# Performance work log

Hardware: AMD Instinct MI355X
Metric: run time of the kernel (lower is better)

## Reference

```python
import jax, jax.numpy as jnp
import numpy as np
import math

EPS_NORM = 1e-12
BN_EPS = 1e-5


def _l2norm(x):
    n = jnp.sqrt(jnp.sum(x * x, axis=-1, keepdims=True))
    return x / jnp.maximum(n, EPS_NORM)


def setup_inputs() -> dict:
    key = jax.random.key(0)
    ks = jax.random.split(key, 16)
    b, c, t, l = 16, 32, 16, 256
    s = 0.05
    return {
        "x": jax.random.normal(ks[0], (b, c, t, l), jnp.float32),
        "q_w": jax.random.normal(ks[1], (c, c), jnp.float32) * s,
        "q_b": jax.random.normal(ks[2], (c,), jnp.float32) * s,
        "k_w": jax.random.normal(ks[3], (c, c), jnp.float32) * s,
        "k_b": jax.random.normal(ks[4], (c,), jnp.float32) * s,
        "v_w": jax.random.normal(ks[5], (c, c), jnp.float32) * s,
        "v_b": jax.random.normal(ks[6], (c,), jnp.float32) * s,
        "m_w": jax.random.normal(ks[7], (c, c), jnp.float32) * s,
        "m_b": jax.random.normal(ks[8], (c,), jnp.float32) * s,
        "pre_prompt": jax.random.normal(ks[9], (1, c, 1, l), jnp.float32) * s,
        "conv_w": jax.random.normal(ks[10], (c, c, 9, 1), jnp.float32) * s,
        "conv_b": jax.random.normal(ks[11], (c,), jnp.float32) * s,
        "bn_gamma": jnp.ones((c,), jnp.float32),
        "bn_beta": jnp.zeros((c,), jnp.float32),
        "lin_w": jax.random.normal(ks[12], (l, l), jnp.float32) * s,
        "lin_b": jax.random.normal(ks[13], (l,), jnp.float32) * s,
        "atten_flag": 1,
    }


def reference(x, q_w, q_b, k_w, k_b, v_w, v_b, m_w, m_b, pre_prompt,
              conv_w, conv_b, bn_gamma, bn_beta, lin_w, lin_b, atten_flag):
    b, c, t, l = x.shape
    nh = 8
    hd = c // nh

    xp = jnp.transpose(x, (0, 2, 3, 1))  # (b,t,l,c)

    def heads(w, bias):
        h = xp @ w.T + bias
        h = h.reshape(b, t, l, nh, hd).transpose(0, 1, 3, 2, 4)  # (b,t,nh,l,hd)
        return _l2norm(h)

    q = heads(q_w, q_b)
    k = heads(k_w, k_b)
    v = heads(v_w, v_b)

    atten = jnp.einsum('bthld,bthmd->bthlm', q, k) / math.sqrt(hd)
    atten = jax.nn.softmax(atten, axis=-1)
    o = jnp.einsum('bthlm,bthmd->bthld', atten, v)  # (b,t,nh,l,hd)
    o = o.transpose(0, 1, 3, 2, 4).reshape(b, t, l, c)
    o = o @ m_w.T + m_b
    xo = jnp.transpose(o, (0, 3, 1, 2))  # (b,c,t,l)

    pre = jnp.broadcast_to(pre_prompt, (b, c, 1, l))
    con = jnp.concatenate([xo[:, :, :8], pre], axis=2)  # (b,c,9,l)

    # ConvNormAct: Conv2d (VALID, kernel (9,1)) + BatchNorm2d (batch stats) + ReLU
    h = jax.lax.conv_general_dilated(
        con, conv_w, window_strides=(1, 1), padding='VALID',
        dimension_numbers=('NCHW', 'OIHW', 'NCHW'))  # (b,c,1,l)
    h = h + conv_b[None, :, None, None]
    mean = jnp.mean(h, axis=(0, 2, 3), keepdims=True)
    var = jnp.var(h, axis=(0, 2, 3), keepdims=True)
    h = (h - mean) * jax.lax.rsqrt(var + BN_EPS)
    h = h * bn_gamma[None, :, None, None] + bn_beta[None, :, None, None]
    h = jax.nn.relu(h)

    p = h @ lin_w.T + lin_b  # Linear over token_len axis
    p = xo[:, :, 2:3] - p
    return jnp.concatenate([xo[:, :, :8], p], axis=2)  # (b,c,9,l)
```

## Files before the change

### kernel.cpp

```cpp
#include <hip/hip_runtime.h>
#include <hip/hip_bf16.h>


#define WF_OFF 0u
#define O_OFF  350080u
#define H_OFF  2447232u
#define S_OFF  2971520u

#define QW   0
#define QB   1024
#define KW   1056
#define KB   2080
#define VW   2112
#define VB   3136
#define MW   3168
#define MB   4192
#define PREo 4224
#define CWo  12416
#define CBo  21632
#define GAMo 21664
#define BETo 21696
#define LWo  21728
#define LBo  87264
#define WF_N 87520

__device__ __forceinline__ int probe_f32(const unsigned short* graw) {
    return graw[0] == 0;
}
__device__ __forceinline__ float ld_any(const void* p, long i, int f32) {
    if (f32) return ((const float*)p)[i];
    union { unsigned int u; float f; } c;
    c.u = ((unsigned int)((const unsigned short*)p)[i]) << 16;
    return c.f;
}
__device__ __forceinline__ void st_out(void* out, size_t i, float v, int f32) {
    if (f32) ((float*)out)[i] = v;
    else ((__hip_bfloat16*)out)[i] = __float2bfloat16(v);
}
__device__ __forceinline__ float ld_out(const void* out, size_t i, int f32) {
    return ld_any(out, (long)i, f32);
}
__device__ __forceinline__ float bflo(unsigned int u) {
    union { unsigned int i; float f; } c; c.i = u << 16; return c.f;
}
__device__ __forceinline__ float bfhi(unsigned int u) {
    union { unsigned int i; float f; } c; c.i = u & 0xffff0000u; return c.f;
}
__device__ __forceinline__ unsigned short f2bs(float f) {
    union { __hip_bfloat16 b; unsigned short s; } c; c.b = __float2bfloat16(f); return c.s;
}
__device__ __forceinline__ unsigned int pk2(float a, float b) {
    return (unsigned int)f2bs(a) | ((unsigned int)f2bs(b) << 16);
}

__global__ __launch_bounds__(256) void k_ingest_p(
    const void* qw, const void* qb, const void* kw, const void* kb,
    const void* vw, const void* vb, const void* mw, const void* mb,
    const void* pre, const void* cw, const void* cb,
    const void* gam, const void* bet, const void* lw, const void* lb,
    float* __restrict__ wf, const unsigned short* __restrict__ graw)
{
    const int f32 = probe_f32(graw);
    const void* srcs[15] = {qw,qb,kw,kb,vw,vb,mw,mb,pre,cw,cb,gam,bet,lw,lb};
    const int starts[16] = {QW,QB,KW,KB,VW,VB,MW,MB,PREo,CWo,CBo,GAMo,BETo,LWo,LBo,WF_N};

    int idx = blockIdx.x * 256 + threadIdx.x;
    if (idx >= WF_N) return;
    int seg = 0;
    #pragma unroll
    for (int j = 1; j < 15; j++) if (idx >= starts[j]) seg = j;
    wf[idx] = ld_any(srcs[seg], idx - starts[seg], f32);
}

__global__ __launch_bounds__(256) void k_attn_fused(
    const void* __restrict__ x, const float* __restrict__ wf,
    unsigned short* __restrict__ O, float* __restrict__ sbuf,
    const unsigned short* __restrict__ graw)
{
    __shared__ uint4 kv[256];
    __shared__ float wgt[3][4][32];
    __shared__ float bia[3][4];

    const int tid = threadIdx.x;
    const int blk = blockIdx.x;
    const int f32 = probe_f32(graw);
    const int h  = blk & 7;
    const int bt = blk >> 3;
    const int b  = bt >> 3, t = bt & 7;

    if (blk == 0 && tid < 64) sbuf[tid] = 0.0f;

    for (int e = tid; e < 384; e += 256) {
        int p = e >> 7, r = e & 127;
        int base = (p == 0) ? QW : ((p == 1) ? KW : VW);
        wgt[p][r >> 5][r & 31] = wf[base + (h * 4 + (r >> 5)) * 32 + (r & 31)];
    }
    if (tid < 12) {
        int p = tid >> 2, r = tid & 3;
        int base = (p == 0) ? QB : ((p == 1) ? KB : VB);
        bia[p][r] = wf[base + h * 4 + r];
    }

    float xv[32];
    const long xbase = ((long)b * 32 * 16 + t) * 256 + tid;
    if (f32) {
        const float* xp = (const float*)x;
        #pragma unroll
        for (int c = 0; c < 32; c++) xv[c] = xp[xbase + (long)c * 4096];
    } else {
        const unsigned short* xp = (const unsigned short*)x;
        #pragma unroll
        for (int c = 0; c < 32; c++) {
            union { unsigned int u; float f; } cc;
            cc.u = ((unsigned int)xp[xbase + (long)c * 4096]) << 16;
            xv[c] = cc.f;
        }
    }

    __syncthreads();

    float4 pr[3];
    #pragma unroll
    for (int p = 0; p < 3; p++) {
        float r0 = bia[p][0], r1 = bia[p][1], r2 = bia[p][2], r3 = bia[p][3];
        #pragma unroll
        for (int c = 0; c < 32; c++) {
            float xc = xv[c];
            r0 = fmaf(xc, wgt[p][0][c], r0);
            r1 = fmaf(xc, wgt[p][1][c], r1);
            r2 = fmaf(xc, wgt[p][2][c], r2);
            r3 = fmaf(xc, wgt[p][3][c], r3);
        }
        float s2 = r0*r0 + r1*r1 + r2*r2 + r3*r3;
        float inv = 1.0f / fmaxf(sqrtf(s2), 1e-12f);
        if (p == 0) inv *= 0.7213475204444817f;
        pr[p] = make_float4(r0*inv, r1*inv, r2*inv, r3*inv);
    }
    kv[tid] = make_uint4(pk2(pr[1].x, pr[1].y), pk2(pr[1].z, pr[1].w),
                         pk2(pr[2].x, pr[2].y), pk2(pr[2].z, pr[2].w));
    float4 q = pr[0];
    __syncthreads();

    float ox = 0.f, oy = 0.f, oz = 0.f, ow = 0.f, den = 0.f;
    #pragma unroll 8
    for (int m = 0; m < 256; m++) {
        uint4 pk = kv[m];
        float s = q.x * bflo(pk.x);
        s = fmaf(q.y, bfhi(pk.x), s);
        s = fmaf(q.z, bflo(pk.y), s);
        s = fmaf(q.w, bfhi(pk.y), s);
        float e = __builtin_amdgcn_exp2f(s);
        den += e;
        ox = fmaf(e, bflo(pk.z), ox);
        oy = fmaf(e, bfhi(pk.z), oy);
        oz = fmaf(e, bflo(pk.w), oz);
        ow = fmaf(e, bfhi(pk.w), ow);
    }
    float inv = 1.0f / den;

    unsigned short us[4] = { f2bs(ox*inv), f2bs(oy*inv), f2bs(oz*inv), f2bs(ow*inv) };
    uint2 opk;
    opk.x = (unsigned int)us[0] | ((unsigned int)us[1] << 16);
    opk.y = (unsigned int)us[2] | ((unsigned int)us[3] << 16);
    *(uint2*)(O + ((size_t)bt * 256u + tid) * 32u + h * 4u) = opk;
}

__global__ __launch_bounds__(256) void k_mproj(
    const unsigned short* __restrict__ O, const float* __restrict__ wf,
    void* __restrict__ out, const unsigned short* __restrict__ graw)
{
    __shared__ float w[1024];
    __shared__ float bias[32];
    const int f32 = probe_f32(graw);
    const int tid = threadIdx.x;
    const int blk = blockIdx.x;
    const int b = blk >> 3, t = blk & 7;

    #pragma unroll
    for (int ii = 0; ii < 4; ii++) w[tid + 256*ii] = wf[MW + tid + 256*ii];
    if (tid < 32) bias[tid] = wf[MB + tid];
    __syncthreads();

    float ov[32];
    const unsigned short* src = O + ((size_t)blk * 256u + tid) * 32u;
    #pragma unroll
    for (int cc = 0; cc < 4; cc++) {
        uint4 u = *(const uint4*)(src + cc * 8);
        unsigned int uu[4] = {u.x, u.y, u.z, u.w};
        #pragma unroll
        for (int j = 0; j < 4; j++) {
            ov[cc*8 + 2*j]     = bflo(uu[j]);
            ov[cc*8 + 2*j + 1] = bfhi(uu[j]);
        }
    }

    for (int co = 0; co < 32; co++) {
        float s = bias[co];
        #pragma unroll
        for (int c = 0; c < 32; c++) s = fmaf(ov[c], w[co*32 + c], s);
        st_out(out, (((size_t)b * 32 + co) * 9 + t) * 256u + tid, s, f32);
    }
}

__global__ __launch_bounds__(256) void k_conv(
    const void* __restrict__ out, const float* __restrict__ wf,
    float* __restrict__ hout, float* __restrict__ s,
    const unsigned short* __restrict__ graw)
{
    __shared__ float w[4][32][9];
    const int f32 = probe_f32(graw);
    const int tid = threadIdx.x;
    const int blk = blockIdx.x;
    const int b = blk >> 3, co0 = (blk & 7) * 4;

    for (int e = tid; e < 1152; e += 256) {
        int g = e / 288, r = e % 288;
        w[g][r / 9][r % 9] = wf[CWo + (co0 + g) * 288 + r];
    }
    __syncthreads();

    const int l = tid;
    float a0 = 0.f, a1 = 0.f, a2 = 0.f, a3 = 0.f;
    for (int ci = 0; ci < 32; ci++) {
        size_t xob = (((size_t)b * 32 + ci) * 9) * 256u + l;
        float pv = wf[PREo + ci * 256 + l];
        #pragma unroll
        for (int kt = 0; kt < 9; kt++) {
            float v = (kt < 8) ? ld_out(out, xob + (size_t)kt * 256u, f32) : pv;
            a0 = fmaf(v, w[0][ci][kt], a0);
            a1 = fmaf(v, w[1][ci][kt], a1);
            a2 = fmaf(v, w[2][ci][kt], a2);
            a3 = fmaf(v, w[3][ci][kt], a3);
        }
    }
    a0 += wf[CBo + co0 + 0]; a1 += wf[CBo + co0 + 1];
    a2 += wf[CBo + co0 + 2]; a3 += wf[CBo + co0 + 3];

    hout[((size_t)b * 32 + co0 + 0) * 256u + l] = a0;
    hout[((size_t)b * 32 + co0 + 1) * 256u + l] = a1;
    hout[((size_t)b * 32 + co0 + 2) * 256u + l] = a2;
    hout[((size_t)b * 32 + co0 + 3) * 256u + l] = a3;

    float acc[4] = {a0, a1, a2, a3};
    #pragma unroll
    for (int g = 0; g < 4; g++) {
        float sg = acc[g], sq = acc[g] * acc[g];
        #pragma unroll
        for (int off = 32; off > 0; off >>= 1) {
            sg += __shfl_down(sg, off, 64);
            sq += __shfl_down(sq, off, 64);
        }
        if ((tid & 63) == 0) {
            atomicAdd(&s[co0 + g], sg);
            atomicAdd(&s[32 + co0 + g], sq);
        }
    }
}

__global__ __launch_bounds__(256) void k_lin(
    const float* __restrict__ hbuf, const float* __restrict__ s,
    const float* __restrict__ wf, void* __restrict__ out,
    const unsigned short* __restrict__ graw)
{
    __shared__ float hn[256];
    const int f32 = probe_f32(graw);
    const int tid = threadIdx.x;
    const int blk = blockIdx.x;
    const int b = blk >> 5, co = blk & 31;

    float mean = s[co] * (1.0f / 4096.0f);
    float var  = fmaxf(s[32 + co] * (1.0f / 4096.0f) - mean * mean, 0.0f);
    float sc = wf[GAMo + co] * __frsqrt_rn(var + 1e-5f);
    float sh = wf[BETo + co] - mean * sc;

    float hv = hbuf[(size_t)blk * 256u + tid];
    hn[tid] = fmaxf(fmaf(hv, sc, sh), 0.0f);
    __syncthreads();

    const float* rp = wf + LWo + (size_t)tid * 256u;
    float acc = 0.f;
    for (int i0 = 0; i0 < 256; i0 += 4) {
        float4 u = *(const float4*)(rp + i0);
        acc = fmaf(hn[i0+0], u.x, acc);
        acc = fmaf(hn[i0+1], u.y, acc);
        acc = fmaf(hn[i0+2], u.z, acc);
        acc = fmaf(hn[i0+3], u.w, acc);
    }
    acc += wf[LBo + tid];

    float xo2 = ld_out(out, (((size_t)b * 32 + co) * 9 + 2) * 256u + tid, f32);
    st_out(out, (((size_t)b * 32 + co) * 9 + 8) * 256u + tid, xo2 - acc, f32);
}

extern "C" void kernel_launch(void* const* d_in, const int* in_sizes, int n_in,
                              void* d_out, int out_size, void* d_ws, size_t ws_size,
                              hipStream_t stream) {
    const unsigned short* graw = (const unsigned short*)d_in[12];

    float* wfp = (float*)((char*)d_ws + WF_OFF);
    unsigned short* Obuf = (unsigned short*)((char*)d_ws + O_OFF);
    float* hbuf = (float*)((char*)d_ws + H_OFF);
    float* sbuf = (float*)((char*)d_ws + S_OFF);

    k_ingest_p  <<<342,  256, 0, stream>>>(d_in[1], d_in[2], d_in[3], d_in[4],
                                           d_in[5], d_in[6], d_in[7], d_in[8],
                                           d_in[9], d_in[10], d_in[11],
                                           d_in[12], d_in[13], d_in[14], d_in[15],
                                           wfp, graw);
    k_attn_fused<<<1024, 256, 0, stream>>>(d_in[0], wfp, Obuf, sbuf, graw);
    k_mproj     <<<128,  256, 0, stream>>>(Obuf, wfp, d_out, graw);
    k_conv      <<<128,  256, 0, stream>>>(d_out, wfp, hbuf, sbuf, graw);
    k_lin       <<<512,  256, 0, stream>>>(hbuf, sbuf, wfp, d_out, graw);
}
```

Baseline: 192.1 us.

## Drop weight ingest kernel, read raw weights directly, two queries per thread

Removes the separate kernel that converted all weights to an fp32 workspace, saving one launch; every later kernel now reads the original weight tensors directly with a dtype switch. The attention kernel runs with 128 threads, each handling two query rows, so every K/V read from shared memory is reused twice. K/V and the intermediate O buffer are now stored as fp16 (round-toward-zero packing) instead of bf16. Weights are no longer staged in shared memory and are instead loaded from global memory inside the inner loops, which may add load pressure. The attention grid also has half as many threads.

```diff
diff --git a/kernel.cpp b/kernel.cpp
--- a/kernel.cpp
+++ b/kernel.cpp
@@ -2,27 +2,11 @@
 #include <hip/hip_bf16.h>
 
 
-#define WF_OFF 0u
-#define O_OFF  350080u
-#define H_OFF  2447232u
-#define S_OFF  2971520u
-
-#define QW   0
-#define QB   1024
-#define KW   1056
-#define KB   2080
-#define VW   2112
-#define VB   3136
-#define MW   3168
-#define MB   4192
-#define PREo 4224
-#define CWo  12416
-#define CBo  21632
-#define GAMo 21664
-#define BETo 21696
-#define LWo  21728
-#define LBo  87264
-#define WF_N 87520
+#define O_OFF  0u
+#define H_OFF  2097152u
+#define S_OFF  2621440u
+
+typedef __fp16 h2 __attribute__((ext_vector_type(2)));
 
 __device__ __forceinline__ int probe_f32(const unsigned short* graw) {
     return graw[0] == 0;
@@ -37,49 +21,28 @@
     if (f32) ((float*)out)[i] = v;
     else ((__hip_bfloat16*)out)[i] = __float2bfloat16(v);
 }
-__device__ __forceinline__ float ld_out(const void* out, size_t i, int f32) {
-    return ld_any(out, (long)i, f32);
-}
 __device__ __forceinline__ float bflo(unsigned int u) {
     union { unsigned int i; float f; } c; c.i = u << 16; return c.f;
 }
 __device__ __forceinline__ float bfhi(unsigned int u) {
     union { unsigned int i; float f; } c; c.i = u & 0xffff0000u; return c.f;
 }
-__device__ __forceinline__ unsigned short f2bs(float f) {
-    union { __hip_bfloat16 b; unsigned short s; } c; c.b = __float2bfloat16(f); return c.s;
-}
-__device__ __forceinline__ unsigned int pk2(float a, float b) {
-    return (unsigned int)f2bs(a) | ((unsigned int)f2bs(b) << 16);
-}
-
-__global__ __launch_bounds__(256) void k_ingest_p(
-    const void* qw, const void* qb, const void* kw, const void* kb,
-    const void* vw, const void* vb, const void* mw, const void* mb,
-    const void* pre, const void* cw, const void* cb,
-    const void* gam, const void* bet, const void* lw, const void* lb,
-    float* __restrict__ wf, const unsigned short* __restrict__ graw)
-{
-    const int f32 = probe_f32(graw);
-    const void* srcs[15] = {qw,qb,kw,kb,vw,vb,mw,mb,pre,cw,cb,gam,bet,lw,lb};
-    const int starts[16] = {QW,QB,KW,KB,VW,VB,MW,MB,PREo,CWo,CBo,GAMo,BETo,LWo,LBo,WF_N};
-
-    int idx = blockIdx.x * 256 + threadIdx.x;
-    if (idx >= WF_N) return;
-    int seg = 0;
-    #pragma unroll
-    for (int j = 1; j < 15; j++) if (idx >= starts[j]) seg = j;
-    wf[idx] = ld_any(srcs[seg], idx - starts[seg], f32);
-}
-
-__global__ __launch_bounds__(256) void k_attn_fused(
-    const void* __restrict__ x, const float* __restrict__ wf,
+__device__ __forceinline__ h2 pkh2(float a, float b) {
+    return __builtin_amdgcn_cvt_pkrtz(a, b);
+}
+
+union KVrow { uint4 u; h2 h[4]; };
+union U4h  { uint4 u; h2 h[4]; };
+
+__global__ __launch_bounds__(128) void k_attn_fused(
+    const void* __restrict__ x,
+    const void* __restrict__ qw, const void* __restrict__ qb,
+    const void* __restrict__ kw, const void* __restrict__ kb,
+    const void* __restrict__ vw, const void* __restrict__ vb,
     unsigned short* __restrict__ O, float* __restrict__ sbuf,
     const unsigned short* __restrict__ graw)
 {
-    __shared__ uint4 kv[256];
-    __shared__ float wgt[3][4][32];
-    __shared__ float bia[3][4];
+    __shared__ uint4 KV[256];
 
     const int tid = threadIdx.x;
     const int blk = blockIdx.x;
@@ -87,154 +50,147 @@
     const int h  = blk & 7;
     const int bt = blk >> 3;
     const int b  = bt >> 3, t = bt & 7;
+    const int h4 = h * 4;
 
     if (blk == 0 && tid < 64) sbuf[tid] = 0.0f;
 
-    for (int e = tid; e < 384; e += 256) {
-        int p = e >> 7, r = e & 127;
-        int base = (p == 0) ? QW : ((p == 1) ? KW : VW);
-        wgt[p][r >> 5][r & 31] = wf[base + (h * 4 + (r >> 5)) * 32 + (r & 31)];
-    }
-    if (tid < 12) {
-        int p = tid >> 2, r = tid & 3;
-        int base = (p == 0) ? QB : ((p == 1) ? KB : VB);
-        bia[p][r] = wf[base + h * 4 + r];
-    }
-
-    float xv[32];
-    const long xbase = ((long)b * 32 * 16 + t) * 256 + tid;
-    if (f32) {
-        const float* xp = (const float*)x;
-        #pragma unroll
-        for (int c = 0; c < 32; c++) xv[c] = xp[xbase + (long)c * 4096];
-    } else {
-        const unsigned short* xp = (const unsigned short*)x;
+    float xv0[32], xv1[32];
+    #pragma unroll
+    for (int c = 0; c < 32; c++) {
+        const long xb = (((long)b * 32 + c) * 16 + t) * 256 + tid;
+        xv0[c] = ld_any(x, xb, f32);
+        xv1[c] = ld_any(x, xb + 128, f32);
+    }
+
+    float4 pr0[3], pr1[3];
+    #pragma unroll
+    for (int p = 0; p < 3; p++) {
+        const void* W = (p == 0) ? qw : ((p == 1) ? kw : vw);
+        const void* B = (p == 0) ? qb : ((p == 1) ? kb : vb);
+        float a0[4], a1[4];
+        #pragma unroll
+        for (int j = 0; j < 4; j++) {
+            float bj = ld_any(B, h4 + j, f32);
+            a0[j] = bj; a1[j] = bj;
+        }
         #pragma unroll
         for (int c = 0; c < 32; c++) {
-            union { unsigned int u; float f; } cc;
-            cc.u = ((unsigned int)xp[xbase + (long)c * 4096]) << 16;
-            xv[c] = cc.f;
-        }
-    }
-
+            float x0 = xv0[c], x1 = xv1[c];
+            #pragma unroll
+            for (int j = 0; j < 4; j++) {
+                float w = ld_any(W, (long)(h4 + j) * 32 + c, f32);
+                a0[j] = fmaf(x0, w, a0[j]);
+                a1[j] = fmaf(x1, w, a1[j]);
+            }
+        }
+        float s20 = a0[0]*a0[0] + a0[1]*a0[1] + a0[2]*a0[2] + a0[3]*a0[3];
+        float s21 = a1[0]*a1[0] + a1[1]*a1[1] + a1[2]*a1[2] + a1[3]*a1[3];
+        float i0 = 1.0f / fmaxf(sqrtf(s20), 1e-12f);
+        float i1 = 1.0f / fmaxf(sqrtf(s21), 1e-12f);
+        if (p == 0) { i0 *= 0.7213475204444817f; i1 *= 0.7213475204444817f; }
+        pr0[p] = make_float4(a0[0]*i0, a0[1]*i0, a0[2]*i0, a0[3]*i0);
+        pr1[p] = make_float4(a1[0]*i1, a1[1]*i1, a1[2]*i1, a1[3]*i1);
+    }
+
+    KVrow r0, r1;
+    r0.h[0] = pkh2(pr0[1].x, pr0[1].y); r0.h[1] = pkh2(pr0[1].z, pr0[1].w);
+    r0.h[2] = pkh2(pr0[2].x, pr0[2].y); r0.h[3] = pkh2(pr0[2].z, pr0[2].w);
+    r1.h[0] = pkh2(pr1[1].x, pr1[1].y); r1.h[1] = pkh2(pr1[1].z, pr1[1].w);
+    r1.h[2] = pkh2(pr1[2].x, pr1[2].y); r1.h[3] = pkh2(pr1[2].z, pr1[2].w);
+    KV[tid]       = r0.u;
+    KV[tid + 128] = r1.u;
+    const float4 qa = pr0[0], qb4 = pr1[0];
     __syncthreads();
 
-    float4 pr[3];
-    #pragma unroll
-    for (int p = 0; p < 3; p++) {
-        float r0 = bia[p][0], r1 = bia[p][1], r2 = bia[p][2], r3 = bia[p][3];
-        #pragma unroll
-        for (int c = 0; c < 32; c++) {
-            float xc = xv[c];
-            r0 = fmaf(xc, wgt[p][0][c], r0);
-            r1 = fmaf(xc, wgt[p][1][c], r1);
-            r2 = fmaf(xc, wgt[p][2][c], r2);
-            r3 = fmaf(xc, wgt[p][3][c], r3);
-        }
-        float s2 = r0*r0 + r1*r1 + r2*r2 + r3*r3;
-        float inv = 1.0f / fmaxf(sqrtf(s2), 1e-12f);
-        if (p == 0) inv *= 0.7213475204444817f;
-        pr[p] = make_float4(r0*inv, r1*inv, r2*inv, r3*inv);
-    }
-    kv[tid] = make_uint4(pk2(pr[1].x, pr[1].y), pk2(pr[1].z, pr[1].w),
-                         pk2(pr[2].x, pr[2].y), pk2(pr[2].z, pr[2].w));
-    float4 q = pr[0];
-    __syncthreads();
-
-    float ox = 0.f, oy = 0.f, oz = 0.f, ow = 0.f, den = 0.f;
+    float o0x=0.f,o0y=0.f,o0z=0.f,o0w=0.f,den0=0.f;
+    float o1x=0.f,o1y=0.f,o1z=0.f,o1w=0.f,den1=0.f;
     #pragma unroll 8
     for (int m = 0; m < 256; m++) {
-        uint4 pk = kv[m];
-        float s = q.x * bflo(pk.x);
-        s = fmaf(q.y, bfhi(pk.x), s);
-        s = fmaf(q.z, bflo(pk.y), s);
-        s = fmaf(q.w, bfhi(pk.y), s);
-        float e = __builtin_amdgcn_exp2f(s);
-        den += e;
-        ox = fmaf(e, bflo(pk.z), ox);
-        oy = fmaf(e, bfhi(pk.z), oy);
-        oz = fmaf(e, bflo(pk.w), oz);
-        ow = fmaf(e, bfhi(pk.w), ow);
-    }
-    float inv = 1.0f / den;
-
-    unsigned short us[4] = { f2bs(ox*inv), f2bs(oy*inv), f2bs(oz*inv), f2bs(ow*inv) };
-    uint2 opk;
-    opk.x = (unsigned int)us[0] | ((unsigned int)us[1] << 16);
-    opk.y = (unsigned int)us[2] | ((unsigned int)us[3] << 16);
-    *(uint2*)(O + ((size_t)bt * 256u + tid) * 32u + h * 4u) = opk;
+        KVrow kv; kv.u = KV[m];
+        float k0 = (float)kv.h[0][0], k1 = (float)kv.h[0][1];
+        float k2 = (float)kv.h[1][0], k3 = (float)kv.h[1][1];
+        float sa = fmaf(qa.x, k0, fmaf(qa.y, k1, fmaf(qa.z, k2, qa.w * k3)));
+        float sb = fmaf(qb4.x, k0, fmaf(qb4.y, k1, fmaf(qb4.z, k2, qb4.w * k3)));
+        float ea = __builtin_amdgcn_exp2f(sa);
+        float eb = __builtin_amdgcn_exp2f(sb);
+        float vx = (float)kv.h[2][0], vy = (float)kv.h[2][1];
+        float vz = (float)kv.h[3][0], vw = (float)kv.h[3][1];
+        den0 += ea; den1 += eb;
+        o0x = fmaf(ea, vx, o0x); o0y = fmaf(ea, vy, o0y);
+        o0z = fmaf(ea, vz, o0z); o0w = fmaf(ea, vw, o0w);
+        o1x = fmaf(eb, vx, o1x); o1y = fmaf(eb, vy, o1y);
+        o1z = fmaf(eb, vz, o1z); o1w = fmaf(eb, vw, o1w);
+    }
+    float i0 = 1.0f / den0, i1 = 1.0f / den1;
+
+    uint2 pk0, pk1;
+    h2 a01 = pkh2(o0x*i0, o0y*i0), a23 = pkh2(o0z*i0, o0w*i0);
+    h2 b01 = pkh2(o1x*i1, o1y*i1), b23 = pkh2(o1z*i1, o1w*i1);
+    pk0.x = *(unsigned int*)&a01; pk0.y = *(unsigned int*)&a23;
+    pk1.x = *(unsigned int*)&b01; pk1.y = *(unsigned int*)&b23;
+    *(uint2*)(O + ((size_t)bt * 256u + tid) * 32u + h4)          = pk0;
+    *(uint2*)(O + ((size_t)bt * 256u + tid + 128) * 32u + h4)    = pk1;
 }
 
 __global__ __launch_bounds__(256) void k_mproj(
-    const unsigned short* __restrict__ O, const float* __restrict__ wf,
+    const unsigned short* __restrict__ O,
+    const void* __restrict__ mw, const void* __restrict__ mb,
     void* __restrict__ out, const unsigned short* __restrict__ graw)
 {
-    __shared__ float w[1024];
-    __shared__ float bias[32];
     const int f32 = probe_f32(graw);
     const int tid = threadIdx.x;
     const int blk = blockIdx.x;
     const int b = blk >> 3, t = blk & 7;
-
-    #pragma unroll
-    for (int ii = 0; ii < 4; ii++) w[tid + 256*ii] = wf[MW + tid + 256*ii];
-    if (tid < 32) bias[tid] = wf[MB + tid];
-    __syncthreads();
 
     float ov[32];
     const unsigned short* src = O + ((size_t)blk * 256u + tid) * 32u;
     #pragma unroll
     for (int cc = 0; cc < 4; cc++) {
-        uint4 u = *(const uint4*)(src + cc * 8);
-        unsigned int uu[4] = {u.x, u.y, u.z, u.w};
+        U4h uu; uu.u = *(const uint4*)(src + cc * 8);
         #pragma unroll
         for (int j = 0; j < 4; j++) {
-            ov[cc*8 + 2*j]     = bflo(uu[j]);
-            ov[cc*8 + 2*j + 1] = bfhi(uu[j]);
+            ov[cc*8 + 2*j]     = (float)uu.h[j][0];
+            ov[cc*8 + 2*j + 1] = (float)uu.h[j][1];
         }
     }
 
     for (int co = 0; co < 32; co++) {
-        float s = bias[co];
-        #pragma unroll
-        for (int c = 0; c < 32; c++) s = fmaf(ov[c], w[co*32 + c], s);
+        float s = ld_any(mb, co, f32);
+        #pragma unroll
+        for (int c = 0; c < 32; c++)
+            s = fmaf(ov[c], ld_any(mw, (long)co * 32 + c, f32), s);
         st_out(out, (((size_t)b * 32 + co) * 9 + t) * 256u + tid, s, f32);
     }
 }
 
 __global__ __launch_bounds__(256) void k_conv(
-    const void* __restrict__ out, const float* __restrict__ wf,
+    const void* __restrict__ out, const void* __restrict__ pre,
+    const void* __restrict__ cw, const void* __restrict__ cb,
     float* __restrict__ hout, float* __restrict__ s,
     const unsigned short* __restrict__ graw)
 {
-    __shared__ float w[4][32][9];
     const int f32 = probe_f32(graw);
     const int tid = threadIdx.x;
     const int blk = blockIdx.x;
     const int b = blk >> 3, co0 = (blk & 7) * 4;
-
-    for (int e = tid; e < 1152; e += 256) {
-        int g = e / 288, r = e % 288;
-        w[g][r / 9][r % 9] = wf[CWo + (co0 + g) * 288 + r];
-    }
-    __syncthreads();
 
     const int l = tid;
     float a0 = 0.f, a1 = 0.f, a2 = 0.f, a3 = 0.f;
     for (int ci = 0; ci < 32; ci++) {
         size_t xob = (((size_t)b * 32 + ci) * 9) * 256u + l;
-        float pv = wf[PREo + ci * 256 + l];
+        float pv = ld_any(pre, (long)ci * 256 + l, f32);
         #pragma unroll
         for (int kt = 0; kt < 9; kt++) {
-            float v = (kt < 8) ? ld_out(out, xob + (size_t)kt * 256u, f32) : pv;
-            a0 = fmaf(v, w[0][ci][kt], a0);
-            a1 = fmaf(v, w[1][ci][kt], a1);
-            a2 = fmaf(v, w[2][ci][kt], a2);
-            a3 = fmaf(v, w[3][ci][kt], a3);
-        }
-    }
-    a0 += wf[CBo + co0 + 0]; a1 += wf[CBo + co0 + 1];
-    a2 += wf[CBo + co0 + 2]; a3 += wf[CBo + co0 + 3];
+            float v = (kt < 8) ? ld_any(out, (long)(xob + (size_t)kt * 256u), f32) : pv;
+            const long wb = (long)ci * 9 + kt;
+            a0 = fmaf(v, ld_any(cw, (long)(co0+0)*288 + wb, f32), a0);
+            a1 = fmaf(v, ld_any(cw, (long)(co0+1)*288 + wb, f32), a1);
+            a2 = fmaf(v, ld_any(cw, (long)(co0+2)*288 + wb, f32), a2);
+            a3 = fmaf(v, ld_any(cw, (long)(co0+3)*288 + wb, f32), a3);
+        }
+    }
+    a0 += ld_any(cb, co0+0, f32); a1 += ld_any(cb, co0+1, f32);
+    a2 += ld_any(cb, co0+2, f32); a3 += ld_any(cb, co0+3, f32);
 
     hout[((size_t)b * 32 + co0 + 0) * 256u + l] = a0;
     hout[((size_t)b * 32 + co0 + 1) * 256u + l] = a1;
@@ -259,8 +215,9 @@
 
 __global__ __launch_bounds__(256) void k_lin(
     const float* __restrict__ hbuf, const float* __restrict__ s,
-    const float* __restrict__ wf, void* __restrict__ out,
-    const unsigned short* __restrict__ graw)
+    const void* __restrict__ gam, const void* __restrict__ bet,
+    const void* __restrict__ lw, const void* __restrict__ lb,
+    void* __restrict__ out, const unsigned short* __restrict__ graw)
 {
     __shared__ float hn[256];
     const int f32 = probe_f32(graw);
@@ -270,25 +227,39 @@
 
     float mean = s[co] * (1.0f / 4096.0f);
     float var  = fmaxf(s[32 + co] * (1.0f / 4096.0f) - mean * mean, 0.0f);
-    float sc = wf[GAMo + co] * __frsqrt_rn(var + 1e-5f);
-    float sh = wf[BETo + co] - mean * sc;
+    float sc = ld_any(gam, co, f32) * __frsqrt_rn(var + 1e-5f);
+    float sh = ld_any(bet, co, f32) - mean * sc;
 
     float hv = hbuf[(size_t)blk * 256u + tid];
     hn[tid] = fmaxf(fmaf(hv, sc, sh), 0.0f);
     __syncthreads();
 
-    const float* rp = wf + LWo + (size_t)tid * 256u;
     float acc = 0.f;
-    for (int i0 = 0; i0 < 256; i0 += 4) {
-        float4 u = *(const float4*)(rp + i0);
-        acc = fmaf(hn[i0+0], u.x, acc);
-        acc = fmaf(hn[i0+1], u.y, acc);
-        acc = fmaf(hn[i0+2], u.z, acc);
-        acc = fmaf(hn[i0+3], u.w, acc);
-    }
-    acc += wf[LBo + tid];
-
-    float xo2 = ld_out(out, (((size_t)b * 32 + co) * 9 + 2) * 256u + tid, f32);
+    if (f32) {
+        const float* rp = (const float*)lw + (size_t)tid * 256u;
+        for (int i0 = 0; i0 < 256; i0 += 4) {
+            float4 u = *(const float4*)(rp + i0);
+            acc = fmaf(hn[i0+0], u.x, acc);
+            acc = fmaf(hn[i0+1], u.y, acc);
+            acc = fmaf(hn[i0+2], u.z, acc);
+            acc = fmaf(hn[i0+3], u.w, acc);
+        }
+    } else {
+        const unsigned short* rp = (const unsigned short*)lw + (size_t)tid * 256u;
+        for (int i0 = 0; i0 < 256; i0 += 16) {
+            uint4 u0 = *(const uint4*)(rp + i0);
+            uint4 u1 = *(const uint4*)(rp + i0 + 8);
+            unsigned int uu[8] = {u0.x, u0.y, u0.z, u0.w, u1.x, u1.y, u1.z, u1.w};
+            #pragma unroll
+            for (int j = 0; j < 8; j++) {
+                acc = fmaf(hn[i0 + 2*j],     bflo(uu[j]), acc);
+                acc = fmaf(hn[i0 + 2*j + 1], bfhi(uu[j]), acc);
+            }
+        }
+    }
+    acc += ld_any(lb, tid, f32);
+
+    float xo2 = ld_any(out, (((long)b * 32 + co) * 9 + 2) * 256 + tid, f32);
     st_out(out, (((size_t)b * 32 + co) * 9 + 8) * 256u + tid, xo2 - acc, f32);
 }
 
@@ -297,18 +268,16 @@
                               hipStream_t stream) {
     const unsigned short* graw = (const unsigned short*)d_in[12];
 
-    float* wfp = (float*)((char*)d_ws + WF_OFF);
     unsigned short* Obuf = (unsigned short*)((char*)d_ws + O_OFF);
     float* hbuf = (float*)((char*)d_ws + H_OFF);
     float* sbuf = (float*)((char*)d_ws + S_OFF);
 
-    k_ingest_p  <<<342,  256, 0, stream>>>(d_in[1], d_in[2], d_in[3], d_in[4],
-                                           d_in[5], d_in[6], d_in[7], d_in[8],
-                                           d_in[9], d_in[10], d_in[11],
-                                           d_in[12], d_in[13], d_in[14], d_in[15],
-                                           wfp, graw);
-    k_attn_fused<<<1024, 256, 0, stream>>>(d_in[0], wfp, Obuf, sbuf, graw);
-    k_mproj     <<<128,  256, 0, stream>>>(Obuf, wfp, d_out, graw);
-    k_conv      <<<128,  256, 0, stream>>>(d_out, wfp, hbuf, sbuf, graw);
-    k_lin       <<<512,  256, 0, stream>>>(hbuf, sbuf, wfp, d_out, graw);
-}
+    k_attn_fused<<<1024, 128, 0, stream>>>(d_in[0], d_in[1], d_in[2], d_in[3],
+                                           d_in[4], d_in[5], d_in[6],
+                                           Obuf, sbuf, graw);
+    k_mproj     <<<128,  256, 0, stream>>>(Obuf, d_in[7], d_in[8], d_out, graw);
+    k_conv      <<<128,  256, 0, stream>>>(d_out, d_in[9], d_in[10], d_in[11],
+                                           hbuf, sbuf, graw);
+    k_lin       <<<512,  256, 0, stream>>>(hbuf, sbuf, d_in[12], d_in[13],
+                                           d_in[14], d_in[15], d_out, graw);
+}
```

Result: slower. 347.7 us (+81.0%).
